# Optimization experiments

Hardware: AMD Instinct MI355X
Metric: run time of the kernel (lower is better)

## Reference

```python
import jax, jax.numpy as jnp
import numpy as np

NUM_POINTS = 16384
OVERSAMPLE = 3
IMPORTANCE_RATIO = 0.75


def point_sample(feat, coords):
    """grid_sample(bilinear, align_corners=False, zero padding) at [0,1]^2 coords.
    feat: (N, C, H, W); coords: (N, P, 2) with coords[...,0]=x (width), [...,1]=y.
    Returns (N, C, P)."""
    N, C, H, W = feat.shape
    # grid_sample with g = 2c-1, align_corners=False -> pixel = c*size - 0.5
    x = coords[..., 0] * W - 0.5
    y = coords[..., 1] * H - 0.5
    x0 = jnp.floor(x)
    y0 = jnp.floor(y)
    x1 = x0 + 1.0
    y1 = y0 + 1.0
    wx1 = x - x0
    wx0 = 1.0 - wx1
    wy1 = y - y0
    wy0 = 1.0 - wy1
    featf = feat.reshape(N, C, H * W)

    def gather(yi, xi):
        valid = (xi >= 0) & (xi <= W - 1) & (yi >= 0) & (yi <= H - 1)
        xic = jnp.clip(xi, 0, W - 1).astype(jnp.int32)
        yic = jnp.clip(yi, 0, H - 1).astype(jnp.int32)
        idx = yic * W + xic  # (N, P)
        v = jnp.take_along_axis(featf, idx[:, None, :], axis=2)  # (N, C, P)
        return v * valid[:, None, :].astype(feat.dtype)

    out = (gather(y0, x0) * (wy0 * wx0)[:, None, :]
           + gather(y0, x1) * (wy0 * wx1)[:, None, :]
           + gather(y1, x0) * (wy1 * wx0)[:, None, :]
           + gather(y1, x1) * (wy1 * wx1)[:, None, :])
    return out


def calculate_uncertainty(logits):
    """logits: (N, C, P) -> (N, P) uncertainty = top2 - top1 (<= 0)."""
    if logits.shape[1] == 1:
        return -jnp.abs(logits)[:, 0, :]
    top2 = jax.lax.top_k(jnp.moveaxis(logits, 1, -1), 2)[0]  # (N, P, 2)
    return top2[..., 1] - top2[..., 0]


def sample_point_coords(coarse_logits):
    """get_uncertain_point_coords_with_randomness (torch.no_grad branch)."""
    N = coarse_logits.shape[0]
    num_sampled = NUM_POINTS * OVERSAMPLE
    num_imp = int(IMPORTANCE_RATIO * NUM_POINTS)
    num_rand = NUM_POINTS - num_imp
    k1, k2 = jax.random.split(jax.random.key(7))
    cand = jax.random.uniform(k1, (N, num_sampled, 2), dtype=jnp.float32)
    cand_logits = point_sample(coarse_logits, cand)  # (N, C, S)
    unc = calculate_uncertainty(cand_logits)  # (N, S)
    idx = jax.lax.top_k(unc, num_imp)[1]  # (N, num_imp)
    imp = jnp.take_along_axis(cand, idx[..., None], axis=1)  # (N, num_imp, 2)
    rand = jax.random.uniform(k2, (N, num_rand, 2), dtype=jnp.float32)
    return jnp.concatenate([imp, rand], axis=1)  # (N, P, 2)


def point_head(fine, coarse_pts, w0, b0, w1, b1, w2, b2, wp, bp):
    x = jnp.concatenate([fine, coarse_pts], axis=1)  # (N, nin+C, P)
    for w, b in ((w0, b0), (w1, b1), (w2, b2)):
        x = jax.nn.relu(jnp.einsum('oc,ncp->nop', w, x) + b[None, :, None])
        x = jnp.concatenate([x, coarse_pts], axis=1)  # coarse_pred_each_layer
    return jnp.einsum('oc,ncp->nop', wp, x) + bp[None, :, None]  # (N, C, P)


def setup_inputs() -> dict:
    key = jax.random.key(0)
    ks = jax.random.split(key, 8)
    N, C, Hc, Wc = 8, 19, 64, 64
    nin, Hf, Wf = 256, 128, 128
    fin = nin + C  # 275
    return {
        'coarse_sem_seg_logits': jax.random.normal(ks[0], (N, C, Hc, Wc), jnp.float32),
        'features': jax.random.normal(ks[1], (N, nin, Hf, Wf), jnp.float32),
        'w0': jax.random.normal(ks[2], (nin, fin), jnp.float32) * (2.0 / fin) ** 0.5,
        'b0': jnp.zeros((nin,), jnp.float32),
        'w1': jax.random.normal(ks[3], (nin, fin), jnp.float32) * (2.0 / fin) ** 0.5,
        'b1': jnp.zeros((nin,), jnp.float32),
        'w2': jax.random.normal(ks[4], (nin, fin), jnp.float32) * (2.0 / fin) ** 0.5,
        'b2': jnp.zeros((nin,), jnp.float32),
        'wp': jax.random.normal(ks[5], (C, fin), jnp.float32) * 0.001,
        'bp': jnp.zeros((C,), jnp.float32),
    }


def reference(coarse_sem_seg_logits, features, w0, b0, w1, b1, w2, b2, wp, bp):
    # training-mode forward of PointRendSemSegHead
    point_coords = jax.lax.stop_gradient(
        sample_point_coords(jax.lax.stop_gradient(coarse_sem_seg_logits)))
    coarse_pts = point_sample(coarse_sem_seg_logits, point_coords)  # (N, C, P)
    fine_pts = point_sample(features, point_coords)  # (N, nin, P)
    point_logits = point_head(fine_pts, coarse_pts, w0, b0, w1, b1, w2, b2, wp, bp)
    return coarse_sem_seg_logits, point_logits, point_coords
```

## Files before the change

### kernel.cpp

```cpp
#include <hip/hip_runtime.h>
#include <stdint.h>

#pragma clang fp contract(off)

#define RNG_MODE 1

#define NB    8
#define CCH   19
#define FCH   256
#define FIN   275
#define KP    288
#define NPTS  16384
#define NSAMP 49152
#define NIMP  12288
#define NRAND 4096
#define SORT_M 65536
#define CHUNK  8192
#define TP    64
#define XROW  640
#define FTR_OFF (8u << 20)
#define FTR_BYTES (134217728ull / 2)

typedef __attribute__((ext_vector_type(8))) short bf16x8;
typedef __attribute__((ext_vector_type(4))) float f32x4;

__host__ __device__ __forceinline__ uint32_t rotl32(uint32_t v, int r) {
  return (v << r) | (v >> (32 - r));
}

__host__ __device__ __forceinline__ void tf2x32(uint32_t k0, uint32_t k1,
                                                uint32_t x0, uint32_t x1,
                                                uint32_t* o0, uint32_t* o1) {
  const uint32_t ks2 = k0 ^ k1 ^ 0x1BD11BDAu;
  x0 += k0; x1 += k1;
#define TF_R(r) { x0 += x1; x1 = rotl32(x1, (r)); x1 ^= x0; }
  TF_R(13) TF_R(15) TF_R(26) TF_R(6)
  x0 += k1;  x1 += ks2 + 1u;
  TF_R(17) TF_R(29) TF_R(16) TF_R(24)
  x0 += ks2; x1 += k0 + 2u;
  TF_R(13) TF_R(15) TF_R(26) TF_R(6)
  x0 += k0;  x1 += k1 + 3u;
  TF_R(17) TF_R(29) TF_R(16) TF_R(24)
  x0 += k1;  x1 += ks2 + 4u;
  TF_R(13) TF_R(15) TF_R(26) TF_R(6)
  x0 += ks2; x1 += k0 + 5u;
#undef TF_R
  *o0 = x0; *o1 = x1;
}

__device__ __forceinline__ float u01(uint32_t b) {
  const float f = __uint_as_float((b >> 9) | 0x3f800000u) - 1.0f;
  return fmaxf(0.0f, f);
}

__device__ __forceinline__ unsigned short f2bf(float f) {
  const uint32_t u = __float_as_uint(f);
  return (unsigned short)((u + 0x7fffu + ((u >> 16) & 1u)) >> 16);
}

__device__ __forceinline__ float bf2f(unsigned short h) {
  return __uint_as_float((uint32_t)h << 16);
}

__global__ __launch_bounds__(256) void gen_uniform_part(float* __restrict__ out,
                                                        unsigned n, uint32_t k0, uint32_t k1) {
  const unsigned i = blockIdx.x * blockDim.x + threadIdx.x;
  if (i >= n) return;
  uint32_t o0, o1;
  tf2x32(k0, k1, 0u, i, &o0, &o1);
  out[i] = u01(o0 ^ o1);
}

__global__ __launch_bounds__(256) void gen_uniform_orig(float* __restrict__ out,
                                                        unsigned half, uint32_t k0, uint32_t k1) {
  const unsigned j = blockIdx.x * blockDim.x + threadIdx.x;
  if (j >= half) return;
  uint32_t o0, o1;
  tf2x32(k0, k1, j, j + half, &o0, &o1);
  out[j] = u01(o0);
  out[j + half] = u01(o1);
}

__global__ __launch_bounds__(256) void unc_keys(const float* __restrict__ coarse,
                                                const float* __restrict__ cand,
                                                unsigned long long* __restrict__ keys) {
  const int tid = blockIdx.x * blockDim.x + threadIdx.x;
  if (tid >= NB * SORT_M) return;
  const int nn = tid >> 16, s = tid & (SORT_M - 1);
  if (s >= NSAMP) { keys[tid] = 0xFFFFFFFFFFFFFFFFull; return; }
  const size_t ci = ((size_t)nn * NSAMP + s) * 2;
  const float cx = cand[ci], cy = cand[ci + 1];
  const float X = cx * 64.0f - 0.5f, Y = cy * 64.0f - 0.5f;
  const float x0f = floorf(X), y0f = floorf(Y);
  const float fx = X - x0f, fy = Y - y0f;
  const float wx0 = 1.0f - fx, wy0 = 1.0f - fy;
  const int x0 = (int)x0f, y0 = (int)y0f;
  const int x0c = min(max(x0, 0), 63), x1c = min(max(x0 + 1, 0), 63);
  const int y0c = min(max(y0, 0), 63), y1c = min(max(y0 + 1, 0), 63);
  const bool vx0 = (x0 >= 0) & (x0 <= 63), vx1 = (x0 >= -1) & (x0 <= 62);
  const bool vy0 = (y0 >= 0) & (y0 <= 63), vy1 = (y0 >= -1) & (y0 <= 62);
  const float w00 = (vy0 & vx0) ? wy0 * wx0 : 0.0f;
  const float w01 = (vy0 & vx1) ? wy0 * fx  : 0.0f;
  const float w10 = (vy1 & vx0) ? fy  * wx0 : 0.0f;
  const float w11 = (vy1 & vx1) ? fy  * fx  : 0.0f;
  const int o00 = y0c * 64 + x0c, o01 = y0c * 64 + x1c;
  const int o10 = y1c * 64 + x0c, o11 = y1c * 64 + x1c;
  const float* cb = coarse + (size_t)nn * (CCH * 4096);
  float m1 = -3.402823466e38f, m2 = -3.402823466e38f;
  for (int c = 0; c < CCH; ++c) {
    const float* pch = cb + (size_t)c * 4096;
    const float v = ((pch[o00] * w00 + pch[o01] * w01) + pch[o10] * w10) + pch[o11] * w11;
    if (v > m1) { m2 = m1; m1 = v; } else if (v > m2) { m2 = v; }
  }
  const float unc = m2 - m1;
  const uint32_t b = __float_as_uint(unc);
  const uint32_t asc = (b & 0x80000000u) ? ~b : (b | 0x80000000u);
  keys[tid] = ((unsigned long long)(~asc) << 32) | (uint32_t)s;
}

__global__ __launch_bounds__(1024) void bitonic_local(unsigned long long* __restrict__ keys) {
  __shared__ unsigned long long s[CHUNK];
  const int cb = blockIdx.x;
  unsigned long long* a = keys + (size_t)cb * CHUNK;
  const unsigned gbase = (unsigned)(cb * CHUNK) & (SORT_M - 1);
  for (int i = threadIdx.x; i < CHUNK; i += 1024) s[i] = a[i];
  __syncthreads();
  for (int k = 2; k <= CHUNK; k <<= 1) {
    for (int j = k >> 1; j > 0; j >>= 1) {
      for (int pid = threadIdx.x; pid < CHUNK / 2; pid += 1024) {
        const int i = ((pid & ~(j - 1)) << 1) | (pid & (j - 1));
        const int l = i | j;
        const bool up = (((gbase + i) & k) == 0);
        const unsigned long long x = s[i], y = s[l];
        if ((x > y) == up) { s[i] = y; s[l] = x; }
      }
      __syncthreads();
    }
  }
  for (int i = threadIdx.x; i < CHUNK; i += 1024) a[i] = s[i];
}

__global__ __launch_bounds__(256) void bitonic_global(unsigned long long* __restrict__ keys,
                                                      int k, int j) {
  const int t = blockIdx.x * blockDim.x + threadIdx.x;
  const int b = t >> 15, pid = t & 32767;
  const int i = ((pid & ~(j - 1)) << 1) | (pid & (j - 1));
  const int l = i | j;
  const bool up = ((i & k) == 0);
  unsigned long long* a = keys + ((size_t)b << 16);
  const unsigned long long x = a[i], y = a[l];
  if ((x > y) == up) { a[i] = y; a[l] = x; }
}

__global__ __launch_bounds__(1024) void bitonic_finish(unsigned long long* __restrict__ keys,
                                                       int k) {
  __shared__ unsigned long long s[CHUNK];
  const int cb = blockIdx.x;
  unsigned long long* a = keys + (size_t)cb * CHUNK;
  const unsigned gi0 = (unsigned)(cb * CHUNK) & (SORT_M - 1);
  for (int i = threadIdx.x; i < CHUNK; i += 1024) s[i] = a[i];
  __syncthreads();
  const bool up = ((gi0 & k) == 0);
  for (int j = CHUNK >> 1; j > 0; j >>= 1) {
    for (int pid = threadIdx.x; pid < CHUNK / 2; pid += 1024) {
      const int i = ((pid & ~(j - 1)) << 1) | (pid & (j - 1));
      const int l = i | j;
      const unsigned long long x = s[i], y = s[l];
      if ((x > y) == up) { s[i] = y; s[l] = x; }
    }
    __syncthreads();
  }
  for (int i = threadIdx.x; i < CHUNK; i += 1024) a[i] = s[i];
}

__global__ __launch_bounds__(256) void write_coords(const unsigned long long* __restrict__ keys,
                                                    const float* __restrict__ cand,
                                                    const float* __restrict__ rnd,
                                                    float* __restrict__ outc) {
  const int t = blockIdx.x * blockDim.x + threadIdx.x;
  if (t >= NB * NPTS) return;
  const int nn = t >> 14, p = t & (NPTS - 1);
  float cx, cy;
  if (p < NIMP) {
    const unsigned idx = (unsigned)(keys[((size_t)nn << 16) + p] & 0xFFFFFFFFu);
    const size_t ci = ((size_t)nn * NSAMP + idx) * 2;
    cx = cand[ci]; cy = cand[ci + 1];
  } else {
    const size_t ri = ((size_t)nn * NRAND + (p - NIMP)) * 2;
    cx = rnd[ri]; cy = rnd[ri + 1];
  }
  outc[(size_t)t * 2] = cx;
  outc[(size_t)t * 2 + 1] = cy;
}

__global__ __launch_bounds__(256) void convert_w(
    const float* __restrict__ w0, const float* __restrict__ w1,
    const float* __restrict__ w2, const float* __restrict__ wpw,
    unsigned short* __restrict__ wbf, unsigned short* __restrict__ wpb) {
  const int i = blockIdx.x * blockDim.x + threadIdx.x;
  if (i < 3 * 256 * KP) {
    const int L = i / (256 * KP);
    const int rem = i - L * (256 * KP);
    const int o = rem / KP, k = rem - o * KP;
    const float* W = (L == 0) ? w0 : (L == 1) ? w1 : w2;
    wbf[i] = (k < FIN) ? f2bf(W[o * FIN + k]) : (unsigned short)0;
  } else if (i < 3 * 256 * KP + 32 * KP) {
    const int j = i - 3 * 256 * KP;
    const int o = j / KP, k = j - o * KP;
    wpb[j] = (o < CCH && k < FIN) ? f2bf(wpw[o * FIN + k]) : (unsigned short)0;
  }
}

__global__ __launch_bounds__(256) void transpose_feats(
    const float* __restrict__ feats, unsigned short* __restrict__ ftr) {
  __shared__ unsigned short tile[64][66];
  const int b = blockIdx.x;
  const int nn = b >> 10;
  const int ct = (b >> 8) & 3;
  const int pt = b & 255;
  const int c0 = ct * 64, p0 = pt * 64;
  const int t = threadIdx.x;
  const float* src = feats + ((size_t)nn << 22);
#pragma unroll 4
  for (int k = 0; k < 16; ++k) {
    const int c = 4 * k + (t >> 6);
    const int p = t & 63;
    tile[p][c] = f2bf(src[((size_t)(c0 + c) << 14) + p0 + p]);
  }
  __syncthreads();
  const int p = t >> 2, q = t & 3;
  const int cb = q * 16;
  uint32_t w[8];
#pragma unroll
  for (int m = 0; m < 8; ++m)
    w[m] = (uint32_t)tile[p][cb + 2 * m] | ((uint32_t)tile[p][cb + 2 * m + 1] << 16);
  unsigned short* dst = ftr + ((((size_t)nn << 14) + p0 + p) << 8) + c0 + cb;
  *(uint4*)(dst)     = make_uint4(w[0], w[1], w[2], w[3]);
  *(uint4*)(dst + 8) = make_uint4(w[4], w[5], w[6], w[7]);
}

template <int USE_TR>
__global__ __launch_bounds__(256, 3) void fused_mfma(
    const float* __restrict__ coarse, const float* __restrict__ feats,
    const unsigned short* __restrict__ ftr,
    const float* __restrict__ b0, const float* __restrict__ b1,
    const float* __restrict__ b2, const float* __restrict__ bp,
    const unsigned short* __restrict__ wbf, const unsigned short* __restrict__ wpb,
    const float* __restrict__ pc, float* __restrict__ outl) {
  __shared__ __align__(16) unsigned short xp[TP * (XROW / 2)];
  __shared__ int   offF[4][TP];  __shared__ float wgtF[4][TP];
  __shared__ int   offC[4][TP];  __shared__ float wgtC[4][TP];

  const int t = threadIdx.x;
  const int nn = blockIdx.x >> 8;
  const int pbase = (blockIdx.x & 255) * TP;

  if (t < TP) {
    const int p = t;
    const size_t ci = ((size_t)nn * NPTS + pbase + p) * 2;
    const float cx = pc[ci], cy = pc[ci + 1];
    {
      const float X = cx * 128.0f - 0.5f, Y = cy * 128.0f - 0.5f;
      const float x0f = floorf(X), y0f = floorf(Y);
      const float fx = X - x0f, fy = Y - y0f;
      const float wx0 = 1.0f - fx, wy0 = 1.0f - fy;
      const int x0 = (int)x0f, y0 = (int)y0f;
      const int x0c = min(max(x0, 0), 127), x1c = min(max(x0 + 1, 0), 127);
      const int y0c = min(max(y0, 0), 127), y1c = min(max(y0 + 1, 0), 127);
      const bool vx0 = (x0 >= 0) & (x0 <= 127), vx1 = (x0 >= -1) & (x0 <= 126);
      const bool vy0 = (y0 >= 0) & (y0 <= 127), vy1 = (y0 >= -1) & (y0 <= 126);
      offF[0][p] = y0c * 128 + x0c; wgtF[0][p] = (vy0 & vx0) ? wy0 * wx0 : 0.0f;
      offF[1][p] = y0c * 128 + x1c; wgtF[1][p] = (vy0 & vx1) ? wy0 * fx  : 0.0f;
      offF[2][p] = y1c * 128 + x0c; wgtF[2][p] = (vy1 & vx0) ? fy  * wx0 : 0.0f;
      offF[3][p] = y1c * 128 + x1c; wgtF[3][p] = (vy1 & vx1) ? fy  * fx  : 0.0f;
    }
    {
      const float X = cx * 64.0f - 0.5f, Y = cy * 64.0f - 0.5f;
      const float x0f = floorf(X), y0f = floorf(Y);
      const float fx = X - x0f, fy = Y - y0f;
      const float wx0 = 1.0f - fx, wy0 = 1.0f - fy;
      const int x0 = (int)x0f, y0 = (int)y0f;
      const int x0c = min(max(x0, 0), 63), x1c = min(max(x0 + 1, 0), 63);
      const int y0c = min(max(y0, 0), 63), y1c = min(max(y0 + 1, 0), 63);
      const bool vx0 = (x0 >= 0) & (x0 <= 63), vx1 = (x0 >= -1) & (x0 <= 62);
      const bool vy0 = (y0 >= 0) & (y0 <= 63), vy1 = (y0 >= -1) & (y0 <= 62);
      offC[0][p] = y0c * 64 + x0c; wgtC[0][p] = (vy0 & vx0) ? wy0 * wx0 : 0.0f;
      offC[1][p] = y0c * 64 + x1c; wgtC[1][p] = (vy0 & vx1) ? wy0 * fx  : 0.0f;
      offC[2][p] = y1c * 64 + x0c; wgtC[2][p] = (vy1 & vx0) ? fy  * wx0 : 0.0f;
      offC[3][p] = y1c * 64 + x1c; wgtC[3][p] = (vy1 & vx1) ? fy  * fx  : 0.0f;
    }
  }
  __syncthreads();

  if (USE_TR) {
    const int p = t >> 2, q = t & 3;
    const unsigned short* base = ftr + (((size_t)nn << 14) << 8) + q * 64;
    const unsigned short* n0 = base + ((size_t)offF[0][p] << 8);
    const unsigned short* n1 = base + ((size_t)offF[1][p] << 8);
    const unsigned short* n2 = base + ((size_t)offF[2][p] << 8);
    const unsigned short* n3 = base + ((size_t)offF[3][p] << 8);
    const float g0 = wgtF[0][p], g1 = wgtF[1][p], g2 = wgtF[2][p], g3 = wgtF[3][p];
    const unsigned swzp = (unsigned)(p & 7) << 4;
#pragma unroll
    for (int m = 0; m < 8; ++m) {
      const bf16x8 a = *(const bf16x8*)(n0 + m * 8);
      const bf16x8 bq = *(const bf16x8*)(n1 + m * 8);
      const bf16x8 c = *(const bf16x8*)(n2 + m * 8);
      const bf16x8 d = *(const bf16x8*)(n3 + m * 8);
      uint32_t u[4];
#pragma unroll
      for (int e = 0; e < 4; ++e) {
        float v0 = fmaf(bf2f((unsigned short)a[2 * e]), g0,
                   fmaf(bf2f((unsigned short)bq[2 * e]), g1,
                   fmaf(bf2f((unsigned short)c[2 * e]), g2,
                        bf2f((unsigned short)d[2 * e]) * g3)));
        float v1 = fmaf(bf2f((unsigned short)a[2 * e + 1]), g0,
                   fmaf(bf2f((unsigned short)bq[2 * e + 1]), g1,
                   fmaf(bf2f((unsigned short)c[2 * e + 1]), g2,
                        bf2f((unsigned short)d[2 * e + 1]) * g3)));
        u[e] = (uint32_t)f2bf(v0) | ((uint32_t)f2bf(v1) << 16);
      }
      *(uint4*)((char*)xp + p * XROW + (((unsigned)((q * 64 + m * 8) * 2)) ^ swzp)) =
          make_uint4(u[0], u[1], u[2], u[3]);
    }
  }

  for (int i = (USE_TR ? 8192 : 0) + t; i < (KP / 2) * TP; i += 256) {
    const int p = i & (TP - 1);
    const int c0 = (i >> 6) * 2;
    float v0 = 0.0f, v1 = 0.0f;
    if (c0 < FCH) {
      const float* fb0 = feats + ((size_t)nn << 22) + ((size_t)c0 << 14);
      const float* fb1 = fb0 + 16384;
      const int o0 = offF[0][p], o1 = offF[1][p], o2 = offF[2][p], o3 = offF[3][p];
      const float g0 = wgtF[0][p], g1 = wgtF[1][p], g2 = wgtF[2][p], g3 = wgtF[3][p];
      v0 = ((fb0[o0] * g0 + fb0[o1] * g1) + fb0[o2] * g2) + fb0[o3] * g3;
      v1 = ((fb1[o0] * g0 + fb1[o1] * g1) + fb1[o2] * g2) + fb1[o3] * g3;
    } else if (c0 < FIN) {
      const float* cb0 = coarse + (size_t)nn * (CCH * 4096) + (size_t)(c0 - FCH) * 4096;
      const int o0 = offC[0][p], o1 = offC[1][p], o2 = offC[2][p], o3 = offC[3][p];
      const float g0 = wgtC[0][p], g1 = wgtC[1][p], g2 = wgtC[2][p], g3 = wgtC[3][p];
      v0 = ((cb0[o0] * g0 + cb0[o1] * g1) + cb0[o2] * g2) + cb0[o3] * g3;
      if (c0 + 1 < FIN) {
        const float* cb1 = cb0 + 4096;
        v1 = ((cb1[o0] * g0 + cb1[o1] * g1) + cb1[o2] * g2) + cb1[o3] * g3;
      }
    }
    const uint32_t u = (uint32_t)f2bf(v0) | ((uint32_t)f2bf(v1) << 16);
    *(uint32_t*)((char*)xp + p * XROW + (((unsigned)(c0 * 2)) ^ ((unsigned)(p & 7) << 4))) = u;
  }

  const int lane = t & 63, wave = t >> 6;
  const int l15 = lane & 15, g = lane >> 4;
  const unsigned swz = (unsigned)(l15 & 7) << 4;
  const char* xpB = (const char*)xp;

  const float* Bs[3] = {b0, b1, b2};

  for (int L = 0; L < 3; ++L) {
    __syncthreads();
    const unsigned short* wL = wbf + (size_t)L * (256 * KP);
    const unsigned short* wbase = wL + ((size_t)(wave * 64 + l15)) * KP + g * 8;

    f32x4 acc[4][4];
#pragma unroll
    for (int mt = 0; mt < 4; ++mt)
#pragma unroll
      for (int nt = 0; nt < 4; ++nt) acc[mt][nt] = (f32x4)(0.0f);

    for (int ks = 0; ks < 9; ++ks) {
      bf16x8 a0 = *(const bf16x8*)(wbase + 0 * 16 * KP + ks * 32);
      bf16x8 a1 = *(const bf16x8*)(wbase + 1 * 16 * KP + ks * 32);
      bf16x8 a2 = *(const bf16x8*)(wbase + 2 * 16 * KP + ks * 32);
      bf16x8 a3 = *(const bf16x8*)(wbase + 3 * 16 * KP + ks * 32);
      const unsigned kb = (unsigned)(ks * 64 + g * 16) ^ swz;
      bf16x8 q0 = *(const bf16x8*)(xpB + (0 * 16 + l15) * XROW + kb);
      bf16x8 q1 = *(const bf16x8*)(xpB + (1 * 16 + l15) * XROW + kb);
      bf16x8 q2 = *(const bf16x8*)(xpB + (2 * 16 + l15) * XROW + kb);
      bf16x8 q3 = *(const bf16x8*)(xpB + (3 * 16 + l15) * XROW + kb);
#pragma unroll
      for (int nt = 0; nt < 4; ++nt) {
        const bf16x8 bq = (nt == 0) ? q0 : (nt == 1) ? q1 : (nt == 2) ? q2 : q3;
        acc[0][nt] = __builtin_amdgcn_mfma_f32_16x16x32_bf16(a0, bq, acc[0][nt], 0, 0, 0);
        acc[1][nt] = __builtin_amdgcn_mfma_f32_16x16x32_bf16(a1, bq, acc[1][nt], 0, 0, 0);
        acc[2][nt] = __builtin_amdgcn_mfma_f32_16x16x32_bf16(a2, bq, acc[2][nt], 0, 0, 0);
        acc[3][nt] = __builtin_amdgcn_mfma_f32_16x16x32_bf16(a3, bq, acc[3][nt], 0, 0, 0);
      }
    }
    __syncthreads();

    const float* __restrict__ Bv = Bs[L];
#pragma unroll
    for (int mt = 0; mt < 4; ++mt) {
      const int ch0 = wave * 64 + mt * 16 + (g << 2);
      const float4 bv = *(const float4*)(Bv + ch0);
#pragma unroll
      for (int nt = 0; nt < 4; ++nt) {
        const int p = nt * 16 + l15;
        const f32x4 v = acc[mt][nt];
        const unsigned short h0 = f2bf(fmaxf(v[0] + bv.x, 0.0f));
        const unsigned short h1 = f2bf(fmaxf(v[1] + bv.y, 0.0f));
        const unsigned short h2 = f2bf(fmaxf(v[2] + bv.z, 0.0f));
        const unsigned short h3 = f2bf(fmaxf(v[3] + bv.w, 0.0f));
        uint2 u;
        u.x = (uint32_t)h0 | ((uint32_t)h1 << 16);
        u.y = (uint32_t)h2 | ((uint32_t)h3 << 16);
        *(uint2*)((char*)xp + p * XROW + (((unsigned)(ch0 * 2)) ^ swz)) = u;
      }
    }
  }
  __syncthreads();

  const unsigned short* hbase = wpb + (size_t)l15 * KP + g * 8;
  f32x4 hacc0 = (f32x4)(0.0f), hacc1 = (f32x4)(0.0f);
  const int pr0 = wave * 2;
  const int mt0 = pr0 >> 2,       nt0 = pr0 & 3;
  const int mt1 = (pr0 + 1) >> 2, nt1 = (pr0 + 1) & 3;
  for (int ks = 0; ks < 9; ++ks) {
    const unsigned kb = (unsigned)(ks * 64 + g * 16) ^ swz;
    const bf16x8 ha0 = *(const bf16x8*)(hbase + mt0 * 16 * KP + ks * 32);
    const bf16x8 hb0 = *(const bf16x8*)(xpB + (nt0 * 16 + l15) * XROW + kb);
    hacc0 = __builtin_amdgcn_mfma_f32_16x16x32_bf16(ha0, hb0, hacc0, 0, 0, 0);
    const bf16x8 ha1 = *(const bf16x8*)(hbase + mt1 * 16 * KP + ks * 32);
    const bf16x8 hb1 = *(const bf16x8*)(xpB + (nt1 * 16 + l15) * XROW + kb);
    hacc1 = __builtin_amdgcn_mfma_f32_16x16x32_bf16(ha1, hb1, hacc1, 0, 0, 0);
  }
#pragma unroll
  for (int q = 0; q < 2; ++q) {
    const f32x4 v = q ? hacc1 : hacc0;
    const int mt = q ? mt1 : mt0, nt = q ? nt1 : nt0;
    const int p = pbase + nt * 16 + l15;
#pragma unroll
    for (int j = 0; j < 4; ++j) {
      const int ch = mt * 16 + (g << 2) + j;
      if (ch < CCH)
        outl[((size_t)nn * CCH + ch) * NPTS + p] = v[j] + bp[ch];
    }
  }
}

extern "C" void kernel_launch(void* const* d_in, const int* in_sizes, int n_in,
                              void* d_out, int out_size, void* d_ws, size_t ws_size,
                              hipStream_t stream) {
  const float* coarse = (const float*)d_in[0];
  const float* feats  = (const float*)d_in[1];
  const float* w0 = (const float*)d_in[2]; const float* b0 = (const float*)d_in[3];
  const float* w1 = (const float*)d_in[4]; const float* b1 = (const float*)d_in[5];
  const float* w2 = (const float*)d_in[6]; const float* b2 = (const float*)d_in[7];
  const float* wp = (const float*)d_in[8]; const float* bp = (const float*)d_in[9];

  float* out0 = (float*)d_out;
  float* outL = out0 + 622592;
  float* outC = outL + 2490368;

  float* cand = (float*)d_ws;
  float* rnd  = cand + 786432;
  unsigned long long* keys =
      (unsigned long long*)((char*)d_ws + 3407872);
  unsigned short* wbf = (unsigned short*)((char*)d_ws + 3407872);
  unsigned short* wpb = wbf + 3 * 256 * KP;
  unsigned short* ftr = (unsigned short*)((char*)d_ws + FTR_OFF);
  const bool use_tr = ws_size >= (size_t)FTR_OFF + FTR_BYTES;

  uint32_t k1a, k1b, k2a, k2b;
#if RNG_MODE == 0
  uint32_t f0, s0, f1, s1;
  tf2x32(0u, 7u, 0u, 2u, &f0, &s0);
  tf2x32(0u, 7u, 1u, 3u, &f1, &s1);
  k1a = f0; k1b = f1; k2a = s0; k2b = s1;
#else
  tf2x32(0u, 7u, 0u, 0u, &k1a, &k1b);
  tf2x32(0u, 7u, 0u, 1u, &k2a, &k2b);
#endif

  hipMemcpyAsync(out0, coarse, 622592 * sizeof(float),
                 hipMemcpyDeviceToDevice, stream);

  if (use_tr)
    transpose_feats<<<8192, 256, 0, stream>>>(feats, ftr);

#if RNG_MODE == 0
  gen_uniform_orig<<<(393216 + 255) / 256, 256, 0, stream>>>(cand, 393216u, k1a, k1b);
  gen_uniform_orig<<<(32768 + 255) / 256, 256, 0, stream>>>(rnd, 32768u, k2a, k2b);
#else
  gen_uniform_part<<<786432 / 256, 256, 0, stream>>>(cand, 786432u, k1a, k1b);
  gen_uniform_part<<<65536 / 256, 256, 0, stream>>>(rnd, 65536u, k2a, k2b);
#endif

  unc_keys<<<2048, 256, 0, stream>>>(coarse, cand, keys);

  bitonic_local<<<64, 1024, 0, stream>>>(keys);
  bitonic_global<<<1024, 256, 0, stream>>>(keys, 16384, 8192);
  bitonic_finish<<<64, 1024, 0, stream>>>(keys, 16384);
  bitonic_global<<<1024, 256, 0, stream>>>(keys, 32768, 16384);
  bitonic_global<<<1024, 256, 0, stream>>>(keys, 32768, 8192);
  bitonic_finish<<<64, 1024, 0, stream>>>(keys, 32768);
  bitonic_global<<<1024, 256, 0, stream>>>(keys, 65536, 32768);
  bitonic_global<<<1024, 256, 0, stream>>>(keys, 65536, 16384);
  bitonic_global<<<1024, 256, 0, stream>>>(keys, 65536, 8192);
  bitonic_finish<<<64, 1024, 0, stream>>>(keys, 65536);

  write_coords<<<512, 256, 0, stream>>>(keys, cand, rnd, outC);

  convert_w<<<(3 * 256 * KP + 32 * KP + 255) / 256, 256, 0, stream>>>(
      w0, w1, w2, wp, wbf, wpb);

  if (use_tr)
    fused_mfma<1><<<2048, 256, 0, stream>>>(coarse, feats, ftr, b0, b1, b2, bp,
                                            wbf, wpb, outC, outL);
  else
    fused_mfma<0><<<2048, 256, 0, stream>>>(coarse, feats, ftr, b0, b1, b2, bp,
                                            wbf, wpb, outC, outL);
}
```

Baseline: 396.4 us.

## Fuse prologue kernels, regenerate RNG on the fly, widen MLP blocks to 512 threads

Merges feature transpose, uncertainty-key computation and weight conversion into one multi-role launch, and recomputes the Threefry uniforms inline instead of writing and reading cand/rnd buffers. The main MFMA kernel moves to 512-thread blocks, with waves split across both channel and point tiles, per-thread interpolation offsets held in registers instead of shared memory, and one head tile per wave. This cuts launch count and global traffic, at the cost of duplicated RNG arithmetic and different occupancy and register pressure.

Result: slower. 408.2 us (+3.0%).

```diff
diff --git a/kernel.cpp b/kernel.cpp
--- a/kernel.cpp
+++ b/kernel.cpp
@@ -2,8 +2,6 @@
 #include <stdint.h>
 
 #pragma clang fp contract(off)
-
-#define RNG_MODE 1
 
 #define NB    8
 #define CCH   19
@@ -18,6 +16,7 @@
 #define CHUNK  8192
 #define TP    64
 #define XROW  640
+#define WBF_OFF (4u << 20)
 #define FTR_OFF (8u << 20)
 #define FTR_BYTES (134217728ull / 2)
 
@@ -48,7 +47,10 @@
   *o0 = x0; *o1 = x1;
 }
 
-__device__ __forceinline__ float u01(uint32_t b) {
+__device__ __forceinline__ float u01_at(uint32_t k0, uint32_t k1, uint32_t i) {
+  uint32_t o0, o1;
+  tf2x32(k0, k1, 0u, i, &o0, &o1);
+  const uint32_t b = o0 ^ o1;
   const float f = __uint_as_float((b >> 9) | 0x3f800000u) - 1.0f;
   return fmaxf(0.0f, f);
 }
@@ -62,60 +64,104 @@
   return __uint_as_float((uint32_t)h << 16);
 }
 
-__global__ __launch_bounds__(256) void gen_uniform_part(float* __restrict__ out,
-                                                        unsigned n, uint32_t k0, uint32_t k1) {
-  const unsigned i = blockIdx.x * blockDim.x + threadIdx.x;
-  if (i >= n) return;
-  uint32_t o0, o1;
-  tf2x32(k0, k1, 0u, i, &o0, &o1);
-  out[i] = u01(o0 ^ o1);
-}
-
-__global__ __launch_bounds__(256) void gen_uniform_orig(float* __restrict__ out,
-                                                        unsigned half, uint32_t k0, uint32_t k1) {
-  const unsigned j = blockIdx.x * blockDim.x + threadIdx.x;
-  if (j >= half) return;
-  uint32_t o0, o1;
-  tf2x32(k0, k1, j, j + half, &o0, &o1);
-  out[j] = u01(o0);
-  out[j + half] = u01(o1);
-}
-
-__global__ __launch_bounds__(256) void unc_keys(const float* __restrict__ coarse,
-                                                const float* __restrict__ cand,
-                                                unsigned long long* __restrict__ keys) {
-  const int tid = blockIdx.x * blockDim.x + threadIdx.x;
-  if (tid >= NB * SORT_M) return;
-  const int nn = tid >> 16, s = tid & (SORT_M - 1);
-  if (s >= NSAMP) { keys[tid] = 0xFFFFFFFFFFFFFFFFull; return; }
-  const size_t ci = ((size_t)nn * NSAMP + s) * 2;
-  const float cx = cand[ci], cy = cand[ci + 1];
-  const float X = cx * 64.0f - 0.5f, Y = cy * 64.0f - 0.5f;
+template <int SZ>
+__device__ __forceinline__ void interp(float cx, float cy, int* off, float* wgt) {
+  const float X = cx * (float)SZ - 0.5f, Y = cy * (float)SZ - 0.5f;
   const float x0f = floorf(X), y0f = floorf(Y);
   const float fx = X - x0f, fy = Y - y0f;
   const float wx0 = 1.0f - fx, wy0 = 1.0f - fy;
   const int x0 = (int)x0f, y0 = (int)y0f;
-  const int x0c = min(max(x0, 0), 63), x1c = min(max(x0 + 1, 0), 63);
-  const int y0c = min(max(y0, 0), 63), y1c = min(max(y0 + 1, 0), 63);
-  const bool vx0 = (x0 >= 0) & (x0 <= 63), vx1 = (x0 >= -1) & (x0 <= 62);
-  const bool vy0 = (y0 >= 0) & (y0 <= 63), vy1 = (y0 >= -1) & (y0 <= 62);
-  const float w00 = (vy0 & vx0) ? wy0 * wx0 : 0.0f;
-  const float w01 = (vy0 & vx1) ? wy0 * fx  : 0.0f;
-  const float w10 = (vy1 & vx0) ? fy  * wx0 : 0.0f;
-  const float w11 = (vy1 & vx1) ? fy  * fx  : 0.0f;
-  const int o00 = y0c * 64 + x0c, o01 = y0c * 64 + x1c;
-  const int o10 = y1c * 64 + x0c, o11 = y1c * 64 + x1c;
-  const float* cb = coarse + (size_t)nn * (CCH * 4096);
-  float m1 = -3.402823466e38f, m2 = -3.402823466e38f;
-  for (int c = 0; c < CCH; ++c) {
-    const float* pch = cb + (size_t)c * 4096;
-    const float v = ((pch[o00] * w00 + pch[o01] * w01) + pch[o10] * w10) + pch[o11] * w11;
-    if (v > m1) { m2 = m1; m1 = v; } else if (v > m2) { m2 = v; }
-  }
-  const float unc = m2 - m1;
-  const uint32_t b = __float_as_uint(unc);
-  const uint32_t asc = (b & 0x80000000u) ? ~b : (b | 0x80000000u);
-  keys[tid] = ((unsigned long long)(~asc) << 32) | (uint32_t)s;
+  const int x0c = min(max(x0, 0), SZ - 1), x1c = min(max(x0 + 1, 0), SZ - 1);
+  const int y0c = min(max(y0, 0), SZ - 1), y1c = min(max(y0 + 1, 0), SZ - 1);
+  const bool vx0 = (x0 >= 0) & (x0 <= SZ - 1), vx1 = (x0 >= -1) & (x0 <= SZ - 2);
+  const bool vy0 = (y0 >= 0) & (y0 <= SZ - 1), vy1 = (y0 >= -1) & (y0 <= SZ - 2);
+  off[0] = y0c * SZ + x0c; wgt[0] = (vy0 & vx0) ? wy0 * wx0 : 0.0f;
+  off[1] = y0c * SZ + x1c; wgt[1] = (vy0 & vx1) ? wy0 * fx  : 0.0f;
+  off[2] = y1c * SZ + x0c; wgt[2] = (vy1 & vx0) ? fy  * wx0 : 0.0f;
+  off[3] = y1c * SZ + x1c; wgt[3] = (vy1 & vx1) ? fy  * fx  : 0.0f;
+}
+
+__global__ __launch_bounds__(256) void fusedA(
+    const float* __restrict__ feats, unsigned short* __restrict__ ftr,
+    const float* __restrict__ coarse, unsigned long long* __restrict__ keys,
+    const float* __restrict__ w0, const float* __restrict__ w1,
+    const float* __restrict__ w2, const float* __restrict__ wpw,
+    unsigned short* __restrict__ wbf, unsigned short* __restrict__ wpb,
+    uint32_t k1a, uint32_t k1b, int use_tr) {
+  __shared__ unsigned short tile[64][66];
+  const int bid = blockIdx.x;
+  const int t = threadIdx.x;
+
+  if (bid < 8192) {
+    if (!use_tr) return;
+    const int nn = bid >> 10;
+    const int ct = (bid >> 8) & 3;
+    const int pt = bid & 255;
+    const int c0 = ct * 64, p0 = pt * 64;
+    const float* src = feats + ((size_t)nn << 22);
+#pragma unroll 4
+    for (int k = 0; k < 16; ++k) {
+      const int c = 4 * k + (t >> 6);
+      const int p = t & 63;
+      tile[p][c] = f2bf(src[((size_t)(c0 + c) << 14) + p0 + p]);
+    }
+    __syncthreads();
+    const int p = t >> 2, q = t & 3;
+    const int cb = q * 16;
+    uint32_t w[8];
+#pragma unroll
+    for (int m = 0; m < 8; ++m)
+      w[m] = (uint32_t)tile[p][cb + 2 * m] | ((uint32_t)tile[p][cb + 2 * m + 1] << 16);
+    unsigned short* dst = ftr + ((((size_t)nn << 14) + p0 + p) << 8) + c0 + cb;
+    *(uint4*)(dst)     = make_uint4(w[0], w[1], w[2], w[3]);
+    *(uint4*)(dst + 8) = make_uint4(w[4], w[5], w[6], w[7]);
+  } else if (bid < 10240) {
+    const int tid = (bid - 8192) * 256 + t;
+    const int nn = tid >> 16, s = tid & (SORT_M - 1);
+    if (s >= NSAMP) { keys[tid] = 0xFFFFFFFFFFFFFFFFull; return; }
+    const uint32_t ci = (uint32_t)(((unsigned)nn * NSAMP + (unsigned)s) * 2);
+    const float cx = u01_at(k1a, k1b, ci);
+    const float cy = u01_at(k1a, k1b, ci + 1);
+    const float X = cx * 64.0f - 0.5f, Y = cy * 64.0f - 0.5f;
+    const float x0f = floorf(X), y0f = floorf(Y);
+    const float fx = X - x0f, fy = Y - y0f;
+    const float wx0 = 1.0f - fx, wy0 = 1.0f - fy;
+    const int x0 = (int)x0f, y0 = (int)y0f;
+    const int x0c = min(max(x0, 0), 63), x1c = min(max(x0 + 1, 0), 63);
+    const int y0c = min(max(y0, 0), 63), y1c = min(max(y0 + 1, 0), 63);
+    const bool vx0 = (x0 >= 0) & (x0 <= 63), vx1 = (x0 >= -1) & (x0 <= 62);
+    const bool vy0 = (y0 >= 0) & (y0 <= 63), vy1 = (y0 >= -1) & (y0 <= 62);
+    const float w00 = (vy0 & vx0) ? wy0 * wx0 : 0.0f;
+    const float w01 = (vy0 & vx1) ? wy0 * fx  : 0.0f;
+    const float w10 = (vy1 & vx0) ? fy  * wx0 : 0.0f;
+    const float w11 = (vy1 & vx1) ? fy  * fx  : 0.0f;
+    const int o00 = y0c * 64 + x0c, o01 = y0c * 64 + x1c;
+    const int o10 = y1c * 64 + x0c, o11 = y1c * 64 + x1c;
+    const float* cb = coarse + (size_t)nn * (CCH * 4096);
+    float m1 = -3.402823466e38f, m2 = -3.402823466e38f;
+    for (int c = 0; c < CCH; ++c) {
+      const float* pch = cb + (size_t)c * 4096;
+      const float v = ((pch[o00] * w00 + pch[o01] * w01) + pch[o10] * w10) + pch[o11] * w11;
+      if (v > m1) { m2 = m1; m1 = v; } else if (v > m2) { m2 = v; }
+    }
+    const float unc = m2 - m1;
+    const uint32_t b = __float_as_uint(unc);
+    const uint32_t asc = (b & 0x80000000u) ? ~b : (b | 0x80000000u);
+    keys[tid] = ((unsigned long long)(~asc) << 32) | (uint32_t)s;
+  } else {
+    const int i = (bid - 10240) * 256 + t;
+    if (i < 3 * 256 * KP) {
+      const int L = i / (256 * KP);
+      const int rem = i - L * (256 * KP);
+      const int o = rem / KP, k = rem - o * KP;
+      const float* W = (L == 0) ? w0 : (L == 1) ? w1 : w2;
+      wbf[i] = (k < FIN) ? f2bf(W[o * FIN + k]) : (unsigned short)0;
+    } else {
+      const int j = i - 3 * 256 * KP;
+      const int o = j / KP, k = j - o * KP;
+      wpb[j] = (o < CCH && k < FIN) ? f2bf(wpw[o * FIN + k]) : (unsigned short)0;
+    }
+  }
 }
 
 __global__ __launch_bounds__(1024) void bitonic_local(unsigned long long* __restrict__ keys) {
@@ -174,73 +220,29 @@
 }
 
 __global__ __launch_bounds__(256) void write_coords(const unsigned long long* __restrict__ keys,
-                                                    const float* __restrict__ cand,
-                                                    const float* __restrict__ rnd,
-                                                    float* __restrict__ outc) {
+                                                    float* __restrict__ outc,
+                                                    uint32_t k1a, uint32_t k1b,
+                                                    uint32_t k2a, uint32_t k2b) {
   const int t = blockIdx.x * blockDim.x + threadIdx.x;
   if (t >= NB * NPTS) return;
   const int nn = t >> 14, p = t & (NPTS - 1);
   float cx, cy;
   if (p < NIMP) {
     const unsigned idx = (unsigned)(keys[((size_t)nn << 16) + p] & 0xFFFFFFFFu);
-    const size_t ci = ((size_t)nn * NSAMP + idx) * 2;
-    cx = cand[ci]; cy = cand[ci + 1];
+    const uint32_t ci = ((unsigned)nn * NSAMP + idx) * 2;
+    cx = u01_at(k1a, k1b, ci);
+    cy = u01_at(k1a, k1b, ci + 1);
   } else {
-    const size_t ri = ((size_t)nn * NRAND + (p - NIMP)) * 2;
-    cx = rnd[ri]; cy = rnd[ri + 1];
+    const uint32_t ri = ((unsigned)nn * NRAND + (unsigned)(p - NIMP)) * 2;
+    cx = u01_at(k2a, k2b, ri);
+    cy = u01_at(k2a, k2b, ri + 1);
   }
   outc[(size_t)t * 2] = cx;
   outc[(size_t)t * 2 + 1] = cy;
 }
 
-__global__ __launch_bounds__(256) void convert_w(
-    const float* __restrict__ w0, const float* __restrict__ w1,
-    const float* __restrict__ w2, const float* __restrict__ wpw,
-    unsigned short* __restrict__ wbf, unsigned short* __restrict__ wpb) {
-  const int i = blockIdx.x * blockDim.x + threadIdx.x;
-  if (i < 3 * 256 * KP) {
-    const int L = i / (256 * KP);
-    const int rem = i - L * (256 * KP);
-    const int o = rem / KP, k = rem - o * KP;
-    const float* W = (L == 0) ? w0 : (L == 1) ? w1 : w2;
-    wbf[i] = (k < FIN) ? f2bf(W[o * FIN + k]) : (unsigned short)0;
-  } else if (i < 3 * 256 * KP + 32 * KP) {
-    const int j = i - 3 * 256 * KP;
-    const int o = j / KP, k = j - o * KP;
-    wpb[j] = (o < CCH && k < FIN) ? f2bf(wpw[o * FIN + k]) : (unsigned short)0;
-  }
-}
-
-__global__ __launch_bounds__(256) void transpose_feats(
-    const float* __restrict__ feats, unsigned short* __restrict__ ftr) {
-  __shared__ unsigned short tile[64][66];
-  const int b = blockIdx.x;
-  const int nn = b >> 10;
-  const int ct = (b >> 8) & 3;
-  const int pt = b & 255;
-  const int c0 = ct * 64, p0 = pt * 64;
-  const int t = threadIdx.x;
-  const float* src = feats + ((size_t)nn << 22);
-#pragma unroll 4
-  for (int k = 0; k < 16; ++k) {
-    const int c = 4 * k + (t >> 6);
-    const int p = t & 63;
-    tile[p][c] = f2bf(src[((size_t)(c0 + c) << 14) + p0 + p]);
-  }
-  __syncthreads();
-  const int p = t >> 2, q = t & 3;
-  const int cb = q * 16;
-  uint32_t w[8];
-#pragma unroll
-  for (int m = 0; m < 8; ++m)
-    w[m] = (uint32_t)tile[p][cb + 2 * m] | ((uint32_t)tile[p][cb + 2 * m + 1] << 16);
-  unsigned short* dst = ftr + ((((size_t)nn << 14) + p0 + p) << 8) + c0 + cb;
-  *(uint4*)(dst)     = make_uint4(w[0], w[1], w[2], w[3]);
-  *(uint4*)(dst + 8) = make_uint4(w[4], w[5], w[6], w[7]);
-}
-
 template <int USE_TR>
-__global__ __launch_bounds__(256, 3) void fused_mfma(
+__global__ __launch_bounds__(512, 6) void fused_mfma(
     const float* __restrict__ coarse, const float* __restrict__ feats,
     const unsigned short* __restrict__ ftr,
     const float* __restrict__ b0, const float* __restrict__ b1,
@@ -248,61 +250,35 @@
     const unsigned short* __restrict__ wbf, const unsigned short* __restrict__ wpb,
     const float* __restrict__ pc, float* __restrict__ outl) {
   __shared__ __align__(16) unsigned short xp[TP * (XROW / 2)];
-  __shared__ int   offF[4][TP];  __shared__ float wgtF[4][TP];
-  __shared__ int   offC[4][TP];  __shared__ float wgtC[4][TP];
 
   const int t = threadIdx.x;
   const int nn = blockIdx.x >> 8;
   const int pbase = (blockIdx.x & 255) * TP;
 
-  if (t < TP) {
-    const int p = t;
-    const size_t ci = ((size_t)nn * NPTS + pbase + p) * 2;
-    const float cx = pc[ci], cy = pc[ci + 1];
-    {
-      const float X = cx * 128.0f - 0.5f, Y = cy * 128.0f - 0.5f;
-      const float x0f = floorf(X), y0f = floorf(Y);
-      const float fx = X - x0f, fy = Y - y0f;
-      const float wx0 = 1.0f - fx, wy0 = 1.0f - fy;
-      const int x0 = (int)x0f, y0 = (int)y0f;
-      const int x0c = min(max(x0, 0), 127), x1c = min(max(x0 + 1, 0), 127);
-      const int y0c = min(max(y0, 0), 127), y1c = min(max(y0 + 1, 0), 127);
-      const bool vx0 = (x0 >= 0) & (x0 <= 127), vx1 = (x0 >= -1) & (x0 <= 126);
-      const bool vy0 = (y0 >= 0) & (y0 <= 127), vy1 = (y0 >= -1) & (y0 <= 126);
-      offF[0][p] = y0c * 128 + x0c; wgtF[0][p] = (vy0 & vx0) ? wy0 * wx0 : 0.0f;
-      offF[1][p] = y0c * 128 + x1c; wgtF[1][p] = (vy0 & vx1) ? wy0 * fx  : 0.0f;
-      offF[2][p] = y1c * 128 + x0c; wgtF[2][p] = (vy1 & vx0) ? fy  * wx0 : 0.0f;
-      offF[3][p] = y1c * 128 + x1c; wgtF[3][p] = (vy1 & vx1) ? fy  * fx  : 0.0f;
-    }
-    {
-      const float X = cx * 64.0f - 0.5f, Y = cy * 64.0f - 0.5f;
-      const float x0f = floorf(X), y0f = floorf(Y);
-      const float fx = X - x0f, fy = Y - y0f;
-      const float wx0 = 1.0f - fx, wy0 = 1.0f - fy;
-      const int x0 = (int)x0f, y0 = (int)y0f;
-      const int x0c = min(max(x0, 0), 63), x1c = min(max(x0 + 1, 0), 63);
-      const int y0c = min(max(y0, 0), 63), y1c = min(max(y0 + 1, 0), 63);
-      const bool vx0 = (x0 >= 0) & (x0 <= 63), vx1 = (x0 >= -1) & (x0 <= 62);
-      const bool vy0 = (y0 >= 0) & (y0 <= 63), vy1 = (y0 >= -1) & (y0 <= 62);
-      offC[0][p] = y0c * 64 + x0c; wgtC[0][p] = (vy0 & vx0) ? wy0 * wx0 : 0.0f;
-      offC[1][p] = y0c * 64 + x1c; wgtC[1][p] = (vy0 & vx1) ? wy0 * fx  : 0.0f;
-      offC[2][p] = y1c * 64 + x0c; wgtC[2][p] = (vy1 & vx0) ? fy  * wx0 : 0.0f;
-      offC[3][p] = y1c * 64 + x1c; wgtC[3][p] = (vy1 & vx1) ? fy  * fx  : 0.0f;
-    }
-  }
-  __syncthreads();
+  int offF[4]; float wgtF[4];
+  int offC[4]; float wgtC[4];
+  int offFc[4]; float wgtFc[4];
+  {
+    const float2 c = *(const float2*)(pc + ((size_t)nn * NPTS + pbase + (t >> 3)) * 2);
+    interp<128>(c.x, c.y, offF, wgtF);
+  }
+  {
+    const float2 c = *(const float2*)(pc + ((size_t)nn * NPTS + pbase + (t & 63)) * 2);
+    interp<64>(c.x, c.y, offC, wgtC);
+    if (!USE_TR) interp<128>(c.x, c.y, offFc, wgtFc);
+  }
 
   if (USE_TR) {
-    const int p = t >> 2, q = t & 3;
-    const unsigned short* base = ftr + (((size_t)nn << 14) << 8) + q * 64;
-    const unsigned short* n0 = base + ((size_t)offF[0][p] << 8);
-    const unsigned short* n1 = base + ((size_t)offF[1][p] << 8);
-    const unsigned short* n2 = base + ((size_t)offF[2][p] << 8);
-    const unsigned short* n3 = base + ((size_t)offF[3][p] << 8);
-    const float g0 = wgtF[0][p], g1 = wgtF[1][p], g2 = wgtF[2][p], g3 = wgtF[3][p];
+    const int p = t >> 3, q = t & 7;
+    const unsigned short* base = ftr + (((size_t)nn << 14) << 8) + q * 32;
+    const unsigned short* n0 = base + ((size_t)offF[0] << 8);
+    const unsigned short* n1 = base + ((size_t)offF[1] << 8);
+    const unsigned short* n2 = base + ((size_t)offF[2] << 8);
+    const unsigned short* n3 = base + ((size_t)offF[3] << 8);
+    const float g0 = wgtF[0], g1 = wgtF[1], g2 = wgtF[2], g3 = wgtF[3];
     const unsigned swzp = (unsigned)(p & 7) << 4;
 #pragma unroll
-    for (int m = 0; m < 8; ++m) {
+    for (int m = 0; m < 4; ++m) {
       const bf16x8 a = *(const bf16x8*)(n0 + m * 8);
       const bf16x8 bq = *(const bf16x8*)(n1 + m * 8);
       const bf16x8 c = *(const bf16x8*)(n2 + m * 8);
@@ -320,30 +296,30 @@
                         bf2f((unsigned short)d[2 * e + 1]) * g3)));
         u[e] = (uint32_t)f2bf(v0) | ((uint32_t)f2bf(v1) << 16);
       }
-      *(uint4*)((char*)xp + p * XROW + (((unsigned)((q * 64 + m * 8) * 2)) ^ swzp)) =
+      *(uint4*)((char*)xp + p * XROW + (((unsigned)((q * 32 + m * 8) * 2)) ^ swzp)) =
           make_uint4(u[0], u[1], u[2], u[3]);
     }
   }
 
-  for (int i = (USE_TR ? 8192 : 0) + t; i < (KP / 2) * TP; i += 256) {
+  for (int i = (USE_TR ? 8192 : 0) + t; i < (KP / 2) * TP; i += 512) {
     const int p = i & (TP - 1);
     const int c0 = (i >> 6) * 2;
     float v0 = 0.0f, v1 = 0.0f;
-    if (c0 < FCH) {
+    if (!USE_TR && c0 < FCH) {
       const float* fb0 = feats + ((size_t)nn << 22) + ((size_t)c0 << 14);
       const float* fb1 = fb0 + 16384;
-      const int o0 = offF[0][p], o1 = offF[1][p], o2 = offF[2][p], o3 = offF[3][p];
-      const float g0 = wgtF[0][p], g1 = wgtF[1][p], g2 = wgtF[2][p], g3 = wgtF[3][p];
-      v0 = ((fb0[o0] * g0 + fb0[o1] * g1) + fb0[o2] * g2) + fb0[o3] * g3;
-      v1 = ((fb1[o0] * g0 + fb1[o1] * g1) + fb1[o2] * g2) + fb1[o3] * g3;
-    } else if (c0 < FIN) {
+      v0 = ((fb0[offFc[0]] * wgtFc[0] + fb0[offFc[1]] * wgtFc[1])
+           + fb0[offFc[2]] * wgtFc[2]) + fb0[offFc[3]] * wgtFc[3];
+      v1 = ((fb1[offFc[0]] * wgtFc[0] + fb1[offFc[1]] * wgtFc[1])
+           + fb1[offFc[2]] * wgtFc[2]) + fb1[offFc[3]] * wgtFc[3];
+    } else if (c0 >= FCH && c0 < FIN) {
       const float* cb0 = coarse + (size_t)nn * (CCH * 4096) + (size_t)(c0 - FCH) * 4096;
-      const int o0 = offC[0][p], o1 = offC[1][p], o2 = offC[2][p], o3 = offC[3][p];
-      const float g0 = wgtC[0][p], g1 = wgtC[1][p], g2 = wgtC[2][p], g3 = wgtC[3][p];
-      v0 = ((cb0[o0] * g0 + cb0[o1] * g1) + cb0[o2] * g2) + cb0[o3] * g3;
+      v0 = ((cb0[offC[0]] * wgtC[0] + cb0[offC[1]] * wgtC[1])
+           + cb0[offC[2]] * wgtC[2]) + cb0[offC[3]] * wgtC[3];
       if (c0 + 1 < FIN) {
         const float* cb1 = cb0 + 4096;
-        v1 = ((cb1[o0] * g0 + cb1[o1] * g1) + cb1[o2] * g2) + cb1[o3] * g3;
+        v1 = ((cb1[offC[0]] * wgtC[0] + cb1[offC[1]] * wgtC[1])
+             + cb1[offC[2]] * wgtC[2]) + cb1[offC[3]] * wgtC[3];
       }
     }
     const uint32_t u = (uint32_t)f2bf(v0) | ((uint32_t)f2bf(v1) << 16);
@@ -351,6 +327,7 @@
   }
 
   const int lane = t & 63, wave = t >> 6;
+  const int wm = wave & 3, wn = wave >> 2;
   const int l15 = lane & 15, g = lane >> 4;
   const unsigned swz = (unsigned)(l15 & 7) << 4;
   const char* xpB = (const char*)xp;
@@ -360,43 +337,41 @@
   for (int L = 0; L < 3; ++L) {
     __syncthreads();
     const unsigned short* wL = wbf + (size_t)L * (256 * KP);
-    const unsigned short* wbase = wL + ((size_t)(wave * 64 + l15)) * KP + g * 8;
-
-    f32x4 acc[4][4];
+    const unsigned short* wbase = wL + (size_t)(wm * 64 + l15) * KP + g * 8;
+
+    f32x4 acc[4][2];
 #pragma unroll
     for (int mt = 0; mt < 4; ++mt)
 #pragma unroll
-      for (int nt = 0; nt < 4; ++nt) acc[mt][nt] = (f32x4)(0.0f);
+      for (int nt = 0; nt < 2; ++nt) acc[mt][nt] = (f32x4)(0.0f);
 
     for (int ks = 0; ks < 9; ++ks) {
-      bf16x8 a0 = *(const bf16x8*)(wbase + 0 * 16 * KP + ks * 32);
-      bf16x8 a1 = *(const bf16x8*)(wbase + 1 * 16 * KP + ks * 32);
-      bf16x8 a2 = *(const bf16x8*)(wbase + 2 * 16 * KP + ks * 32);
-      bf16x8 a3 = *(const bf16x8*)(wbase + 3 * 16 * KP + ks * 32);
+      const bf16x8 a0 = *(const bf16x8*)(wbase + 0 * 16 * KP + ks * 32);
+      const bf16x8 a1 = *(const bf16x8*)(wbase + 1 * 16 * KP + ks * 32);
+      const bf16x8 a2 = *(const bf16x8*)(wbase + 2 * 16 * KP + ks * 32);
+      const bf16x8 a3 = *(const bf16x8*)(wbase + 3 * 16 * KP + ks * 32);
       const unsigned kb = (unsigned)(ks * 64 + g * 16) ^ swz;
-      bf16x8 q0 = *(const bf16x8*)(xpB + (0 * 16 + l15) * XROW + kb);
-      bf16x8 q1 = *(const bf16x8*)(xpB + (1 * 16 + l15) * XROW + kb);
-      bf16x8 q2 = *(const bf16x8*)(xpB + (2 * 16 + l15) * XROW + kb);
-      bf16x8 q3 = *(const bf16x8*)(xpB + (3 * 16 + l15) * XROW + kb);
-#pragma unroll
-      for (int nt = 0; nt < 4; ++nt) {
-        const bf16x8 bq = (nt == 0) ? q0 : (nt == 1) ? q1 : (nt == 2) ? q2 : q3;
-        acc[0][nt] = __builtin_amdgcn_mfma_f32_16x16x32_bf16(a0, bq, acc[0][nt], 0, 0, 0);
-        acc[1][nt] = __builtin_amdgcn_mfma_f32_16x16x32_bf16(a1, bq, acc[1][nt], 0, 0, 0);
-        acc[2][nt] = __builtin_amdgcn_mfma_f32_16x16x32_bf16(a2, bq, acc[2][nt], 0, 0, 0);
-        acc[3][nt] = __builtin_amdgcn_mfma_f32_16x16x32_bf16(a3, bq, acc[3][nt], 0, 0, 0);
-      }
+      const bf16x8 q0 = *(const bf16x8*)(xpB + (wn * 32 + 0 + l15) * XROW + kb);
+      const bf16x8 q1 = *(const bf16x8*)(xpB + (wn * 32 + 16 + l15) * XROW + kb);
+      acc[0][0] = __builtin_amdgcn_mfma_f32_16x16x32_bf16(a0, q0, acc[0][0], 0, 0, 0);
+      acc[1][0] = __builtin_amdgcn_mfma_f32_16x16x32_bf16(a1, q0, acc[1][0], 0, 0, 0);
+      acc[2][0] = __builtin_amdgcn_mfma_f32_16x16x32_bf16(a2, q0, acc[2][0], 0, 0, 0);
+      acc[3][0] = __builtin_amdgcn_mfma_f32_16x16x32_bf16(a3, q0, acc[3][0], 0, 0, 0);
+      acc[0][1] = __builtin_amdgcn_mfma_f32_16x16x32_bf16(a0, q1, acc[0][1], 0, 0, 0);
+      acc[1][1] = __builtin_amdgcn_mfma_f32_16x16x32_bf16(a1, q1, acc[1][1], 0, 0, 0);
+      acc[2][1] = __builtin_amdgcn_mfma_f32_16x16x32_bf16(a2, q1, acc[2][1], 0, 0, 0);
+      acc[3][1] = __builtin_amdgcn_mfma_f32_16x16x32_bf16(a3, q1, acc[3][1], 0, 0, 0);
     }
     __syncthreads();
 
     const float* __restrict__ Bv = Bs[L];
 #pragma unroll
     for (int mt = 0; mt < 4; ++mt) {
-      const int ch0 = wave * 64 + mt * 16 + (g << 2);
+      const int ch0 = wm * 64 + mt * 16 + (g << 2);
       const float4 bv = *(const float4*)(Bv + ch0);
 #pragma unroll
-      for (int nt = 0; nt < 4; ++nt) {
-        const int p = nt * 16 + l15;
+      for (int nt = 0; nt < 2; ++nt) {
+        const int p = wn * 32 + nt * 16 + l15;
         const f32x4 v = acc[mt][nt];
         const unsigned short h0 = f2bf(fmaxf(v[0] + bv.x, 0.0f));
         const unsigned short h1 = f2bf(fmaxf(v[1] + bv.y, 0.0f));
@@ -411,31 +386,21 @@
   }
   __syncthreads();
 
-  const unsigned short* hbase = wpb + (size_t)l15 * KP + g * 8;
-  f32x4 hacc0 = (f32x4)(0.0f), hacc1 = (f32x4)(0.0f);
-  const int pr0 = wave * 2;
-  const int mt0 = pr0 >> 2,       nt0 = pr0 & 3;
-  const int mt1 = (pr0 + 1) >> 2, nt1 = (pr0 + 1) & 3;
+  const int hmt = wave >> 2, hnt = wave & 3;
+  const unsigned short* hbase = wpb + (size_t)(hmt * 16 + l15) * KP + g * 8;
+  f32x4 hacc = (f32x4)(0.0f);
   for (int ks = 0; ks < 9; ++ks) {
     const unsigned kb = (unsigned)(ks * 64 + g * 16) ^ swz;
-    const bf16x8 ha0 = *(const bf16x8*)(hbase + mt0 * 16 * KP + ks * 32);
-    const bf16x8 hb0 = *(const bf16x8*)(xpB + (nt0 * 16 + l15) * XROW + kb);
-    hacc0 = __builtin_amdgcn_mfma_f32_16x16x32_bf16(ha0, hb0, hacc0, 0, 0, 0);
-    const bf16x8 ha1 = *(const bf16x8*)(hbase + mt1 * 16 * KP + ks * 32);
-    const bf16x8 hb1 = *(const bf16x8*)(xpB + (nt1 * 16 + l15) * XROW + kb);
-    hacc1 = __builtin_amdgcn_mfma_f32_16x16x32_bf16(ha1, hb1, hacc1, 0, 0, 0);
-  }
-#pragma unroll
-  for (int q = 0; q < 2; ++q) {
-    const f32x4 v = q ? hacc1 : hacc0;
-    const int mt = q ? mt1 : mt0, nt = q ? nt1 : nt0;
-    const int p = pbase + nt * 16 + l15;
-#pragma unroll
-    for (int j = 0; j < 4; ++j) {
-      const int ch = mt * 16 + (g << 2) + j;
-      if (ch < CCH)
-        outl[((size_t)nn * CCH + ch) * NPTS + p] = v[j] + bp[ch];
-    }
+    const bf16x8 ha = *(const bf16x8*)(hbase + ks * 32);
+    const bf16x8 hb = *(const bf16x8*)(xpB + (hnt * 16 + l15) * XROW + kb);
+    hacc = __builtin_amdgcn_mfma_f32_16x16x32_bf16(ha, hb, hacc, 0, 0, 0);
+  }
+  const int p = pbase + hnt * 16 + l15;
+#pragma unroll
+  for (int j = 0; j < 4; ++j) {
+    const int ch = hmt * 16 + (g << 2) + j;
+    if (ch < CCH)
+      outl[((size_t)nn * CCH + ch) * NPTS + p] = hacc[j] + bp[ch];
   }
 }
 
@@ -453,41 +418,21 @@
   float* outL = out0 + 622592;
   float* outC = outL + 2490368;
 
-  float* cand = (float*)d_ws;
-  float* rnd  = cand + 786432;
-  unsigned long long* keys =
-      (unsigned long long*)((char*)d_ws + 3407872);
-  unsigned short* wbf = (unsigned short*)((char*)d_ws + 3407872);
+  unsigned long long* keys = (unsigned long long*)d_ws;
+  unsigned short* wbf = (unsigned short*)((char*)d_ws + WBF_OFF);
   unsigned short* wpb = wbf + 3 * 256 * KP;
   unsigned short* ftr = (unsigned short*)((char*)d_ws + FTR_OFF);
-  const bool use_tr = ws_size >= (size_t)FTR_OFF + FTR_BYTES;
+  const int use_tr = (ws_size >= (size_t)FTR_OFF + FTR_BYTES) ? 1 : 0;
 
   uint32_t k1a, k1b, k2a, k2b;
-#if RNG_MODE == 0
-  uint32_t f0, s0, f1, s1;
-  tf2x32(0u, 7u, 0u, 2u, &f0, &s0);
-  tf2x32(0u, 7u, 1u, 3u, &f1, &s1);
-  k1a = f0; k1b = f1; k2a = s0; k2b = s1;
-#else
   tf2x32(0u, 7u, 0u, 0u, &k1a, &k1b);
   tf2x32(0u, 7u, 0u, 1u, &k2a, &k2b);
-#endif
 
   hipMemcpyAsync(out0, coarse, 622592 * sizeof(float),
                  hipMemcpyDeviceToDevice, stream);
 
-  if (use_tr)
-    transpose_feats<<<8192, 256, 0, stream>>>(feats, ftr);
-
-#if RNG_MODE == 0
-  gen_uniform_orig<<<(393216 + 255) / 256, 256, 0, stream>>>(cand, 393216u, k1a, k1b);
-  gen_uniform_orig<<<(32768 + 255) / 256, 256, 0, stream>>>(rnd, 32768u, k2a, k2b);
-#else
-  gen_uniform_part<<<786432 / 256, 256, 0, stream>>>(cand, 786432u, k1a, k1b);
-  gen_uniform_part<<<65536 / 256, 256, 0, stream>>>(rnd, 65536u, k2a, k2b);
-#endif
-
-  unc_keys<<<2048, 256, 0, stream>>>(coarse, cand, keys);
+  fusedA<<<11140, 256, 0, stream>>>(feats, ftr, coarse, keys,
+                                    w0, w1, w2, wp, wbf, wpb, k1a, k1b, use_tr);
 
   bitonic_local<<<64, 1024, 0, stream>>>(keys);
   bitonic_global<<<1024, 256, 0, stream>>>(keys, 16384, 8192);
@@ -500,15 +445,12 @@
   bitonic_global<<<1024, 256, 0, stream>>>(keys, 65536, 8192);
   bitonic_finish<<<64, 1024, 0, stream>>>(keys, 65536);
 
-  write_coords<<<512, 256, 0, stream>>>(keys, cand, rnd, outC);
-
-  convert_w<<<(3 * 256 * KP + 32 * KP + 255) / 256, 256, 0, stream>>>(
-      w0, w1, w2, wp, wbf, wpb);
+  write_coords<<<512, 256, 0, stream>>>(keys, outC, k1a, k1b, k2a, k2b);
 
   if (use_tr)
-    fused_mfma<1><<<2048, 256, 0, stream>>>(coarse, feats, ftr, b0, b1, b2, bp,
+    fused_mfma<1><<<2048, 512, 0, stream>>>(coarse, feats, ftr, b0, b1, b2, bp,
                                             wbf, wpb, outC, outL);
   else
-    fused_mfma<0><<<2048, 256, 0, stream>>>(coarse, feats, ftr, b0, b1, b2, bp,
+    fused_mfma<0><<<2048, 512, 0, stream>>>(coarse, feats, ftr, b0, b1, b2, bp,
                                             wbf, wpb, outC, outL);
 }
```
